# Optimization experiments

Hardware: AMD Instinct MI355X
Metric: run time of the kernel (lower is better)

Reference implementation:

```python
import jax, jax.numpy as jnp
import numpy as np

BATCH = 4096
FEAT = 4096

def setup_inputs() -> dict:
    key = jax.random.key(0)
    k1, k2, k3 = jax.random.split(key, 3)
    out1 = jax.random.normal(k1, (BATCH, FEAT), dtype=jnp.float32)
    out2 = jax.random.normal(k2, (BATCH, FEAT), dtype=jnp.float32)
    out3 = jax.random.normal(k3, (BATCH, FEAT), dtype=jnp.float32)
    return {"out1": out1, "out2": out2, "out3": out3}

def reference(out1, out2, out3):
    # per-sample L2 distances (torch.dist(a, b, 2) over the feature dim)
    d13 = jnp.sqrt(jnp.sum((out1 - out3) ** 2, axis=-1))  # [B]
    d12 = jnp.sqrt(jnp.sum((out1 - out2) ** 2, axis=-1))  # [B]
    compare = 2.0 - d13 + d12                              # [B]
    # Faithful to original: torch.max(zeros(B,1), compare[B]) broadcasts to [B,B]
    B = compare.shape[0]
    hinged = jnp.maximum(jnp.zeros((B, 1), dtype=compare.dtype), compare)  # [B,B]
    return jnp.sum(hinged)
```

## Files before the change

### kernel.cpp

```cpp
#include <hip/hip_runtime.h>
#include <math.h>

#define FEAT 4096
#define BATCH 4096

__global__ __launch_bounds__(256) void row_dist_kernel(
    const float* __restrict__ o1, const float* __restrict__ o2,
    const float* __restrict__ o3, float* __restrict__ row_out)
{
    const int row = blockIdx.x;
    const int tid = threadIdx.x;
    const float4* p1 = (const float4*)(o1 + (size_t)row * FEAT);
    const float4* p2 = (const float4*)(o2 + (size_t)row * FEAT);
    const float4* p3 = (const float4*)(o3 + (size_t)row * FEAT);

    float s13 = 0.0f, s12 = 0.0f;
    #pragma unroll
    for (int k = 0; k < 4; ++k) {
        const int idx = tid + k * 256;
        const float4 a = p1[idx];
        const float4 b = p2[idx];
        const float4 c = p3[idx];
        float d;
        d = a.x - c.x; s13 += d * d;
        d = a.y - c.y; s13 += d * d;
        d = a.z - c.z; s13 += d * d;
        d = a.w - c.w; s13 += d * d;
        d = a.x - b.x; s12 += d * d;
        d = a.y - b.y; s12 += d * d;
        d = a.z - b.z; s12 += d * d;
        d = a.w - b.w; s12 += d * d;
    }

    #pragma unroll
    for (int off = 32; off > 0; off >>= 1) {
        s13 += __shfl_down(s13, off, 64);
        s12 += __shfl_down(s12, off, 64);
    }

    __shared__ float ls13[4];
    __shared__ float ls12[4];
    const int wave = tid >> 6;
    const int lane = tid & 63;
    if (lane == 0) { ls13[wave] = s13; ls12[wave] = s12; }
    __syncthreads();
    if (tid == 0) {
        const float t13 = ls13[0] + ls13[1] + ls13[2] + ls13[3];
        const float t12 = ls12[0] + ls12[1] + ls12[2] + ls12[3];
        const float compare = 2.0f - sqrtf(t13) + sqrtf(t12);
        row_out[row] = fmaxf(compare, 0.0f);
    }
}

__global__ __launch_bounds__(1024) void final_reduce_kernel(
    const float* __restrict__ row_vals, float* __restrict__ out)
{
    const int tid = threadIdx.x;
    float s = 0.0f;
    #pragma unroll
    for (int k = 0; k < BATCH / 1024; ++k) s += row_vals[tid + k * 1024];

    #pragma unroll
    for (int off = 32; off > 0; off >>= 1) s += __shfl_down(s, off, 64);

    __shared__ float ls[16];
    const int wave = tid >> 6;
    const int lane = tid & 63;
    if (lane == 0) ls[wave] = s;
    __syncthreads();
    if (tid == 0) {
        float t = 0.0f;
        #pragma unroll
        for (int i = 0; i < 16; ++i) t += ls[i];
        out[0] = t * (float)BATCH;
    }
}

extern "C" void kernel_launch(void* const* d_in, const int* in_sizes, int n_in,
                              void* d_out, int out_size, void* d_ws, size_t ws_size,
                              hipStream_t stream) {
    const float* o1 = (const float*)d_in[0];
    const float* o2 = (const float*)d_in[1];
    const float* o3 = (const float*)d_in[2];
    float* row_ws = (float*)d_ws;
    float* out = (float*)d_out;

    row_dist_kernel<<<BATCH, 256, 0, stream>>>(o1, o2, o3, row_ws);
    final_reduce_kernel<<<1, 1024, 0, stream>>>(row_ws, out);
}
```

Measured before the change: 189.9 us.

## Assign one wavefront per row and drop block-level shared reduction

Each 64-lane wavefront now handles a whole row, with four rows per 256-thread block, so the grid shrinks to a quarter of the blocks. This removes the shared-memory cross-wave reduction and the __syncthreads. The inner loop processes two float4 groups per iteration with split accumulators, giving more independent loads in flight per lane. Per-lane register pressure rises and fewer blocks are launched, but the kernel stays bound by memory bandwidth over 192 MB of input.

```diff
diff --git a/kernel.cpp b/kernel.cpp
--- a/kernel.cpp
+++ b/kernel.cpp
@@ -3,34 +3,47 @@
 
 #define FEAT 4096
 #define BATCH 4096
+#define WPB 4
+#define NBLK (BATCH / WPB)
 
 __global__ __launch_bounds__(256) void row_dist_kernel(
     const float* __restrict__ o1, const float* __restrict__ o2,
     const float* __restrict__ o3, float* __restrict__ row_out)
 {
-    const int row = blockIdx.x;
-    const int tid = threadIdx.x;
+    const int tid  = threadIdx.x;
+    const int wave = tid >> 6;
+    const int lane = tid & 63;
+    const int row  = blockIdx.x * WPB + wave;
+
     const float4* p1 = (const float4*)(o1 + (size_t)row * FEAT);
     const float4* p2 = (const float4*)(o2 + (size_t)row * FEAT);
     const float4* p3 = (const float4*)(o3 + (size_t)row * FEAT);
 
-    float s13 = 0.0f, s12 = 0.0f;
+    float s13a = 0.f, s12a = 0.f, s13b = 0.f, s12b = 0.f;
+
     #pragma unroll
-    for (int k = 0; k < 4; ++k) {
-        const int idx = tid + k * 256;
-        const float4 a = p1[idx];
-        const float4 b = p2[idx];
-        const float4 c = p3[idx];
+    for (int g = 0; g < 8; ++g) {
+        const int i0 = lane + (2 * g + 0) * 64;
+        const int i1 = lane + (2 * g + 1) * 64;
+        const float4 a0 = p1[i0];
+        const float4 c0 = p3[i0];
+        const float4 b0 = p2[i0];
+        const float4 a1 = p1[i1];
+        const float4 c1 = p3[i1];
+        const float4 b1 = p2[i1];
         float d;
-        d = a.x - c.x; s13 += d * d;
-        d = a.y - c.y; s13 += d * d;
-        d = a.z - c.z; s13 += d * d;
-        d = a.w - c.w; s13 += d * d;
-        d = a.x - b.x; s12 += d * d;
-        d = a.y - b.y; s12 += d * d;
-        d = a.z - b.z; s12 += d * d;
-        d = a.w - b.w; s12 += d * d;
+        d = a0.x - c0.x; s13a += d * d;  d = a0.y - c0.y; s13a += d * d;
+        d = a0.z - c0.z; s13a += d * d;  d = a0.w - c0.w; s13a += d * d;
+        d = a0.x - b0.x; s12a += d * d;  d = a0.y - b0.y; s12a += d * d;
+        d = a0.z - b0.z; s12a += d * d;  d = a0.w - b0.w; s12a += d * d;
+        d = a1.x - c1.x; s13b += d * d;  d = a1.y - c1.y; s13b += d * d;
+        d = a1.z - c1.z; s13b += d * d;  d = a1.w - c1.w; s13b += d * d;
+        d = a1.x - b1.x; s12b += d * d;  d = a1.y - b1.y; s12b += d * d;
+        d = a1.z - b1.z; s12b += d * d;  d = a1.w - b1.w; s12b += d * d;
     }
+
+    float s13 = s13a + s13b;
+    float s12 = s12a + s12b;
 
     #pragma unroll
     for (int off = 32; off > 0; off >>= 1) {
@@ -38,16 +51,8 @@
         s12 += __shfl_down(s12, off, 64);
     }
 
-    __shared__ float ls13[4];
-    __shared__ float ls12[4];
-    const int wave = tid >> 6;
-    const int lane = tid & 63;
-    if (lane == 0) { ls13[wave] = s13; ls12[wave] = s12; }
-    __syncthreads();
-    if (tid == 0) {
-        const float t13 = ls13[0] + ls13[1] + ls13[2] + ls13[3];
-        const float t12 = ls12[0] + ls12[1] + ls12[2] + ls12[3];
-        const float compare = 2.0f - sqrtf(t13) + sqrtf(t12);
+    if (lane == 0) {
+        const float compare = 2.0f - sqrtf(s13) + sqrtf(s12);
         row_out[row] = fmaxf(compare, 0.0f);
     }
 }
@@ -85,6 +90,6 @@
     float* row_ws = (float*)d_ws;
     float* out = (float*)d_out;
 
-    row_dist_kernel<<<BATCH, 256, 0, stream>>>(o1, o2, o3, row_ws);
+    row_dist_kernel<<<NBLK, 256, 0, stream>>>(o1, o2, o3, row_ws);
     final_reduce_kernel<<<1, 1024, 0, stream>>>(row_ws, out);
 }
```

Result: slower. 196.0 us (+3.2%).
